# Optimization experiments

Measured on AMD Instinct MI355X. Metric: run time of the kernel, lower is better.

## Reference

```python
import jax, jax.numpy as jnp
import numpy as np

CUTOFF = 10.0
K = 32            # max_num_neighbors
NUM_GRAPHS = 64
ATOMS = 128
N = NUM_GRAPHS * ATOMS
HID = 128
FIL = 128
NG = 50           # num_gaussians
LAYERS = 6
MAX_Z = 100
PI = 3.14159265   # constant used verbatim in the torch source


def silu(x):
    return x * jax.nn.sigmoid(x)


def build_graph(pos, batch):
    """Dense cdist + per-node top-K neighbor selection (radius_graph_pure).
    Returns idx[i,k] = k-th nearest neighbor j of center i, and a validity mask.
    Torch edge (row, col) = (j, i): node j receives a message computed from x[i].
    """
    p = jax.lax.stop_gradient(pos)
    d2 = jnp.sum((p[:, None, :] - p[None, :, :]) ** 2, -1)          # [N,N]
    same = batch[:, None] == batch[None, :]
    eye = jnp.eye(p.shape[0], dtype=bool)
    valid = same & (d2 < CUTOFF * CUTOFF) & (~eye)
    dm = jnp.where(valid, d2, jnp.inf)
    neg, idx = jax.lax.top_k(-dm, K)                                 # [N,K]
    return idx, jnp.isfinite(neg)                                    # edge valid iff within mask


def setup_inputs() -> dict:
    key = jax.random.key(0)
    ks = jax.random.split(key, 20)
    s = 0.05
    inp = {
        "pos": jax.random.normal(ks[0], (N, 3), jnp.float32),
        "z": jax.random.randint(ks[1], (N,), 0, MAX_Z),
        "batch": jnp.repeat(jnp.arange(NUM_GRAPHS), ATOMS),
        # parameters (weights stored as [in, out])
        "emb": jax.random.normal(ks[2], (MAX_Z, HID), jnp.float32) * s,
        "mw1": jax.random.normal(ks[3], (LAYERS, NG, FIL), jnp.float32) * s,
        "mb1": jax.random.normal(ks[4], (LAYERS, FIL), jnp.float32) * s,
        "mw2": jax.random.normal(ks[5], (LAYERS, FIL, FIL), jnp.float32) * s,
        "mb2": jax.random.normal(ks[6], (LAYERS, FIL), jnp.float32) * s,
        "l1w": jax.random.normal(ks[7], (LAYERS, HID, FIL), jnp.float32) * s,
        "l1b": jax.random.normal(ks[8], (LAYERS, FIL), jnp.float32) * s,
        "l2w": jax.random.normal(ks[9], (LAYERS, FIL, HID), jnp.float32) * s,
        "l2b": jax.random.normal(ks[10], (LAYERS, HID), jnp.float32) * s,
        "ow1": jax.random.normal(ks[11], (HID, HID // 2), jnp.float32) * s,
        "ob1": jax.random.normal(ks[12], (HID // 2,), jnp.float32) * s,
        "ow2": jax.random.normal(ks[13], (HID // 2, 1), jnp.float32) * s,
        "ob2": jax.random.normal(ks[14], (1,), jnp.float32) * s,
    }
    return inp


def reference(pos, z, batch, emb, mw1, mb1, mw2, mb2, l1w, l1b, l2w, l2b, ow1, ob1, ow2, ob2):
    idx, evalid = build_graph(pos, batch)                 # [N,K], [N,K]
    ev = evalid.astype(pos.dtype)
    diff = pos[idx] - pos[:, None, :]                     # [N,K,3]
    d2e = jnp.sum(diff * diff, -1)
    dist = jnp.sqrt(jnp.where(evalid, d2e, 1.0))          # safe sqrt for masked edges
    offset = jnp.linspace(0.0, CUTOFF, NG)
    width = CUTOFF / (NG - 1)
    rbf = jnp.exp(-0.5 * ((dist[..., None] - offset) / width) ** 2)   # [N,K,NG]
    cval = 0.5 * (jnp.cos(dist * PI / CUTOFF) + 1.0)
    cval = cval * (dist < CUTOFF).astype(pos.dtype) * ev  # zero out invalid edges

    h = emb[z]                                            # [N,HID]
    flat_idx = idx.reshape(-1)                            # receivers (torch row)
    for l in range(LAYERS):
        W = silu(rbf @ mw1[l] + mb1[l]) @ mw2[l] + mb2[l]           # filter MLP
        W = W * cval[..., None]                                       # [N,K,FIL]
        xj = (h @ l1w[l] + l1b[l])[:, None, :]                        # sender = center i
        msg = (xj * W).reshape(N * K, FIL)
        agg = jax.ops.segment_sum(msg, flat_idx, num_segments=N)     # scatter_add at row
        h = h + silu(agg @ l2w[l] + l2b[l])

    out = (silu(h @ ow1 + ob1) @ ow2 + ob2)[:, 0]         # [N]
    return jax.ops.segment_sum(out, batch, num_segments=NUM_GRAPHS)  # [G]
```

## Files before the change

### kernel.cpp

```cpp
#include <hip/hip_runtime.h>
#include <math.h>

typedef unsigned short u16;
typedef unsigned int   u32;
typedef unsigned long long u64;

#define NATOMS 8192
#define GRAPHS 64
#define KNN    32
#define NGAUSS 50
#define HID    128
#define LAYERS 6
#define NTAB   4096
#define SA     136
#define SW1    72
#define SH     132

typedef __attribute__((ext_vector_type(8))) short bf16x8;
typedef __attribute__((ext_vector_type(4))) float f32x4;

__device__ __forceinline__ float bf2f(u16 v) {
    return __uint_as_float(((u32)v) << 16);
}
__device__ __forceinline__ u16 f2bf(float f) {
    u32 u = __float_as_uint(f);
    u32 lsb = (u >> 16) & 1u;
    u += 0x7fffu + lsb;
    return (u16)(u >> 16);
}
__device__ __forceinline__ u32 pkbf(float lo, float hi) {
#if __has_builtin(__builtin_amdgcn_cvt_pk_bf16_f32)
    auto r = __builtin_amdgcn_cvt_pk_bf16_f32(lo, hi);
    u32 u; __builtin_memcpy(&u, &r, 4); return u;
#else
    return (u32)f2bf(lo) | ((u32)f2bf(hi) << 16);
#endif
}
__device__ __forceinline__ float silu_f(float x) {
    return x * __builtin_amdgcn_rcpf(1.0f + __expf(-x));
}
__device__ __forceinline__ bf16x8 ldfrag(const u16* p) {
    return *(const bf16x8*)__builtin_assume_aligned(p, 16);
}
__device__ __forceinline__ u64 shfl_xor_u64(u64 v, int mask) {
    u32 lo = (u32)v, hi = (u32)(v >> 32);
    lo = (u32)__shfl_xor((int)lo, mask, 64);
    hi = (u32)__shfl_xor((int)hi, mask, 64);
    return ((u64)hi << 32) | lo;
}
__device__ __forceinline__ float ldf(const void* p, int i, bool f32in) {
    return f32in ? ((const float*)p)[i] : bf2f(((const u16*)p)[i]);
}
union U8 { bf16x8 v; u32 w[4]; };

__global__ void probe_kernel(const u16* __restrict__ raw, int* __restrict__ flag,
                             int* __restrict__ rev_cnt, float* __restrict__ gsum,
                             int* __restrict__ done_cnt, int* __restrict__ xflags) {
    __shared__ int s;
    int t = threadIdx.x;
    if (t == 0) s = 0;
    __syncthreads();
    float x = bf2f(raw[2 * t]);
    if (!(fabsf(x) < 1000.0f)) atomicOr(&s, 1);
    for (int i = t; i < NATOMS; i += 256) rev_cnt[i] = 0;
    for (int i = t; i < 2048; i += 256) xflags[i] = 0;
    if (t < GRAPHS) gsum[t] = 0.0f;
    if (t == 0) *done_cnt = 0;
    __syncthreads();
    if (t == 0) *flag = s;
}

#define NARR 9
struct IngestDesc {
    const void* src[NARR];
    void*       dst[NARR];
    int         n[NARR];
};

#define NB_BUILD 2048
#define NB_PREP  768

__launch_bounds__(256)
__global__ void setup_kernel(const void* __restrict__ pos,
                             const void* __restrict__ l1w, const void* __restrict__ l2w,
                             u16* __restrict__ l1wt, u16* __restrict__ l2wt,
                             IngestDesc d, int total_ing,
                             const int* __restrict__ flag,
                             int* __restrict__ rev_cnt, u32* __restrict__ rev) {
    int bid = blockIdx.x;
    bool f32in = (*flag != 0);
    if (bid < NB_BUILD) {
        int wv = threadIdx.x >> 6, lane = threadIdx.x & 63;
        int t = bid * 4 + wv;
        int tl = t & 127;
        int base = t & ~127;
        float cx = ldf(pos, t * 3 + 0, f32in);
        float cy = ldf(pos, t * 3 + 1, f32in);
        float cz = ldf(pos, t * 3 + 2, f32in);
        u64 key[2];
#pragma unroll
        for (int c = 0; c < 2; ++c) {
            int j = lane + c * 64;
            float jx = ldf(pos, (base + j) * 3 + 0, f32in);
            float jy = ldf(pos, (base + j) * 3 + 1, f32in);
            float jz = ldf(pos, (base + j) * 3 + 2, f32in);
            float dx = __fsub_rn(cx, jx);
            float dy = __fsub_rn(cy, jy);
            float dz = __fsub_rn(cz, jz);
            float d2 = __fadd_rn(__fadd_rn(__fmul_rn(dx, dx), __fmul_rn(dy, dy)),
                                 __fmul_rn(dz, dz));
            bool valid = (j != tl) && (d2 < 100.0f);
            key[c] = valid ? ((((u64)__float_as_uint(d2)) << 32) | (u32)j) : ~0ULL;
        }
#pragma unroll
        for (int k = 2; k <= 128; k <<= 1) {
#pragma unroll
            for (int j = k >> 1; j > 0; j >>= 1) {
                if (j == 64) {
                    u64 lo = key[0] < key[1] ? key[0] : key[1];
                    u64 hi = key[0] < key[1] ? key[1] : key[0];
                    key[0] = lo; key[1] = hi;
                } else {
#pragma unroll
                    for (int r = 0; r < 2; ++r) {
                        u64 o = shfl_xor_u64(key[r], j);
                        u32 ii = (u32)(r * 64 + lane);
                        bool dir = ((ii & (u32)k) == 0);
                        bool lower = ((ii & (u32)j) == 0);
                        bool keep_min = (dir == lower);
                        bool less = key[r] < o;
                        key[r] = (less == keep_min) ? key[r] : o;
                    }
                }
            }
        }
        if (lane < KNN) {
            u64 m = key[0];
            if (m != ~0ULL) {
                float d2 = __uint_as_float((u32)(m >> 32));
                float dd = __fsqrt_rn(d2);
                if (dd < 10.0f) {
                    float u = dd * ((float)(NTAB - 1) / 10.0f);
                    int i0 = (int)(u + 0.5f);
                    if (i0 > NTAB - 1) i0 = NTAB - 1;
                    int jn = base + (int)(m & 0xffffffffu);
                    int p = atomicAdd(&rev_cnt[jn], 1);
                    rev[(size_t)jn * 128 + p] = ((u32)i0 << 7) | (u32)(t & 127);
                }
            }
        }
    } else if (bid < NB_BUILD + NB_PREP) {
        int gid = (bid - NB_BUILD) * 256 + threadIdx.x;
        int seg = gid / 98304;
        int tt = gid % 98304;
        int l = tt >> 14;
        int n = (tt >> 7) & 127;
        int k = tt & 127;
        const void* src = (seg == 0) ? l1w : l2w;
        u16* dst = (seg == 0) ? l1wt : l2wt;
        int si = l * 16384 + k * 128 + n;
        float v = f32in ? ((const float*)src)[si] : bf2f(((const u16*)src)[si]);
        dst[tt] = f2bf(v);
    } else {
        int gid = (bid - NB_BUILD - NB_PREP) * 256 + threadIdx.x;
        if (gid < total_ing) {
            int a = 0, off = gid;
            while (off >= d.n[a]) { off -= d.n[a]; ++a; }
            float v = f32in ? ((const float*)d.src[a])[off]
                            : bf2f(((const u16*)d.src[a])[off]);
            ((float*)d.dst[a])[off] = v;
        }
    }
}

__launch_bounds__(256)
__global__ void vtab_kernel(const void* __restrict__ mw1,
                            const void* __restrict__ mw2,
                            const float* __restrict__ b1,
                            const float* __restrict__ b2,
                            const int* __restrict__ flag,
                            u32* __restrict__ pk) {
    __shared__ u16 s_t1[128 * SA];
    __shared__ u16 s_w1[128 * SW1];
    __shared__ u16 s_w2[128 * SA];
    int tid = threadIdx.x;
    int l = blockIdx.x / (NTAB / 128);
    int rbase = (blockIdx.x % (NTAB / 128)) * 128;
    {
        bool f32in = (*flag != 0);
#pragma unroll
        for (int p = 0; p < 32; ++p) {
            int idx = p * 256 + tid;
            int k = idx >> 7, n = idx & 127;
            float v = (k < 50) ? ldf(mw1, l * 6400 + k * 128 + n, f32in) : 0.0f;
            s_w1[n * SW1 + k] = f2bf(v);
        }
#pragma unroll
        for (int p = 0; p < 64; ++p) {
            int idx = p * 256 + tid;
            int k = idx >> 7, n = idx & 127;
            s_w2[n * SA + k] = f2bf(ldf(mw2, l * 16384 + k * 128 + n, f32in));
        }
    }
    __syncthreads();

    int wv = tid >> 6, lane = tid & 63;
    int quad = lane >> 4, lr = lane & 15;
    int m0 = wv * 32;

    {
        const float wgi = 49.0f / 10.0f;
        const float dstep = 10.0f / (float)(NTAB - 1);
        U8 afr[2][2];
#pragma unroll
        for (int mt = 0; mt < 2; ++mt) {
            float d = (float)(rbase + m0 + mt * 16 + lr) * dstep;
            float u = d * wgi;
#pragma unroll
            for (int kki = 0; kki < 2; ++kki) {
                float t0 = u - (float)(quad * 8) - (float)(kki * 32);
                float vj[8];
#pragma unroll
                for (int j = 0; j < 8; ++j) {
                    float tt = t0 - (float)j;
                    float e = __expf(-0.5f * tt * tt);
                    if (kki == 1 && (quad * 8 + j) >= 18) e = 0.0f;
                    vj[j] = e;
                }
#pragma unroll
                for (int p = 0; p < 4; ++p)
                    afr[mt][kki].w[p] = pkbf(vj[2 * p], vj[2 * p + 1]);
            }
        }
        f32x4 accA[2][8];
#pragma unroll
        for (int mt = 0; mt < 2; ++mt)
#pragma unroll
            for (int nt = 0; nt < 8; ++nt) accA[mt][nt] = (f32x4){0.f, 0.f, 0.f, 0.f};
#pragma unroll
        for (int kki = 0; kki < 2; ++kki) {
#pragma unroll
            for (int nt = 0; nt < 8; ++nt) {
                bf16x8 b = ldfrag(&s_w1[(nt * 16 + lr) * SW1 + kki * 32 + quad * 8]);
                accA[0][nt] = __builtin_amdgcn_mfma_f32_16x16x32_bf16(afr[0][kki].v, b, accA[0][nt], 0, 0, 0);
                accA[1][nt] = __builtin_amdgcn_mfma_f32_16x16x32_bf16(afr[1][kki].v, b, accA[1][nt], 0, 0, 0);
            }
        }
#pragma unroll
        for (int mt = 0; mt < 2; ++mt) {
            int r0 = m0 + mt * 16 + quad * 4;
            u16* tp0 = &s_t1[r0 * SA + lr];
#pragma unroll
            for (int nt = 0; nt < 8; ++nt) {
                int col = nt * 16;
                float bb = b1[l * 128 + col + lr];
                u32 p01 = pkbf(silu_f(accA[mt][nt][0] + bb),
                               silu_f(accA[mt][nt][1] + bb));
                u32 p23 = pkbf(silu_f(accA[mt][nt][2] + bb),
                               silu_f(accA[mt][nt][3] + bb));
                u16* tp = tp0 + col;
                tp[0]      = (u16)p01;
                tp[SA]     = (u16)(p01 >> 16);
                tp[2 * SA] = (u16)p23;
                tp[3 * SA] = (u16)(p23 >> 16);
            }
        }
    }
    {
        f32x4 accB[2][8];
#pragma unroll
        for (int mt = 0; mt < 2; ++mt)
#pragma unroll
            for (int nt = 0; nt < 8; ++nt) accB[mt][nt] = (f32x4){0.f, 0.f, 0.f, 0.f};
#pragma unroll
        for (int kk = 0; kk < 128; kk += 32) {
            bf16x8 a0 = ldfrag(&s_t1[(m0 + lr)      * SA + kk + quad * 8]);
            bf16x8 a1 = ldfrag(&s_t1[(m0 + 16 + lr) * SA + kk + quad * 8]);
#pragma unroll
            for (int nt = 0; nt < 8; ++nt) {
                bf16x8 b = ldfrag(&s_w2[(nt * 16 + lr) * SA + kk + quad * 8]);
                accB[0][nt] = __builtin_amdgcn_mfma_f32_16x16x32_bf16(a0, b, accB[0][nt], 0, 0, 0);
                accB[1][nt] = __builtin_amdgcn_mfma_f32_16x16x32_bf16(a1, b, accB[1][nt], 0, 0, 0);
            }
        }
        const float dstep = 10.0f / (float)(NTAB - 1);
#pragma unroll
        for (int mt = 0; mt < 2; ++mt) {
            int r0 = m0 + mt * 16 + quad * 4;
            float cv[4];
#pragma unroll
            for (int r = 0; r < 4; ++r) {
                float d = (float)(rbase + r0 + r) * dstep;
                cv[r] = 0.5f * (cosf(d * 3.14159265f / 10.0f) + 1.0f);
            }
#pragma unroll
            for (int nt = 0; nt < 8; ++nt) {
                int col = nt * 16 + lr;
                float bb = b2[l * 128 + col];
#pragma unroll
                for (int r = 0; r < 4; ++r) {
                    float val = (accB[mt][nt][r] + bb) * cv[r];
                    float oth = __shfl_xor(val, 1, 64);
                    if ((lr & 1) == 0) {
                        int row = rbase + r0 + r;
                        pk[((size_t)l * NTAB + row) * 64 + (col >> 1)] =
                            pkbf(val, oth);
                    }
                }
            }
        }
    }
}

#define AGG_ISSUE(T, X, base, ev)                                              \
    {                                                                          \
        _Pragma("unroll") for (int q = 0; q < 8; ++q) {                        \
            int e = (base) + q;                                                \
            u32 pe = __builtin_amdgcn_readlane((ev), e & 63);                  \
            int sy = (int)(pe >> 7);                                           \
            int sx = (int)(pe & 127u);                                         \
            T[q] = pkl[(size_t)sy * 64 + lane];                                \
            X[q] = *(const u32*)&s_x[sx * SA + c2];                            \
        }                                                                      \
    }

#define AGG_COMPUTE(T, X)                                                      \
    {                                                                          \
        _Pragma("unroll") for (int q = 0; q < 8; ++q) {                        \
            float v0 = bf2f((u16)T[q]) * bf2f((u16)X[q]);                      \
            float v1 = bf2f((u16)(T[q] >> 16)) * bf2f((u16)(X[q] >> 16));      \
            switch (q & 3) {                                                   \
                case 0: a0 += v0; a1 += v1; break;                             \
                case 1: b0 += v0; b1v += v1; break;                            \
                case 2: c0 += v0; c1 += v1; break;                             \
                default: d0 += v0; d1 += v1; break;                            \
            }                                                                  \
        }                                                                      \
    }

__launch_bounds__(1024, 1)
__global__ void graph_kernel(const int* __restrict__ rev_cnt,
                             const u32* __restrict__ rev,
                             const u32* __restrict__ pk,
                             const int* __restrict__ z,
                             const float* __restrict__ emb,
                             const u16* __restrict__ l1wt,
                             const float* __restrict__ l1b,
                             const u16* __restrict__ l2wt,
                             const float* __restrict__ l2b,
                             const float* __restrict__ ow1,
                             const float* __restrict__ ob1,
                             const float* __restrict__ ow2,
                             const float* __restrict__ ob2,
                             u32* __restrict__ xbuf,
                             int* __restrict__ xflags,
                             float* __restrict__ gsum,
                             int* __restrict__ done_cnt,
                             void* __restrict__ out,
                             const int* __restrict__ flag) {
    __shared__ __align__(16) u16 s_x[128 * SA];
    __shared__ __align__(16) u16 s_hb[64 * SA];
    __shared__ __align__(16) u16 s_pair[2 * 64 * SA];
    __shared__ float s_b1a[LAYERS * 128];
    __shared__ float s_b2a[LAYERS * 128];
    __shared__ float s_sum;
    __shared__ int s_last;

    u16* s_ahi = s_pair;
    u16* s_alo = s_pair + 64 * SA;

    int tid = threadIdx.x;
    int bid = blockIdx.x;
    int g = bid & 63, q4 = bid >> 6;
    int abase = g * 128;
    int rbase = q4 * 32;
    int w = tid >> 6, lane = tid & 63;
    int quad = lane >> 4, lr = lane & 15;
    int rowt = (w >> 3) * 16;
    int coln = (w & 7) * 16;
    int c2 = lane * 2;

    float hreg[4];

    for (int i = tid; i < LAYERS * 128; i += 1024) {
        s_b1a[i] = l1b[i];
        s_b2a[i] = l2b[i];
    }

    int j0 = abase + rbase + w * 2;
    int dgv[2];
    u32 eAv[2], eBv[2];
#pragma unroll
    for (int rr = 0; rr < 2; ++rr) {
        int j = j0 + rr;
        dgv[rr] = rev_cnt[j];
        eAv[rr] = rev[(size_t)j * 128 + lane];
        eBv[rr] = (dgv[rr] > 64) ? rev[(size_t)j * 128 + 64 + lane] : eAv[rr];
    }

    {
        int r = tid >> 5, cb = (tid & 31) * 4;
        const float* src = emb + (size_t)z[abase + rbase + r] * 128 + cb;
        float4 v = *(const float4*)src;
        u32* dd = (u32*)&s_hb[r * SA + cb];
        dd[0] = pkbf(v.x, v.y); dd[1] = pkbf(v.z, v.w);
    }
    __syncthreads();

    {
        f32x4 acc = (f32x4){0.f, 0.f, 0.f, 0.f};
#pragma unroll
        for (int kk = 0; kk < 128; kk += 32) {
            bf16x8 a = ldfrag(&s_hb[(rowt + lr) * SA + kk + quad * 8]);
            bf16x8 b = ldfrag(l1wt + (coln + lr) * 128 + kk + quad * 8);
            acc = __builtin_amdgcn_mfma_f32_16x16x32_bf16(a, b, acc, 0, 0, 0);
        }
#pragma unroll
        for (int r = 0; r < 4; ++r) {
            int col = coln + lr;
            s_x[(rbase + rowt + quad * 4 + r) * SA + col] =
                f2bf(acc[r] + s_b1a[col]);
        }
    }

    for (int l = 0; l <= LAYERS; ++l) {
        if (l < LAYERS) {
            int e = l;
            u32* xbw = xbuf + ((size_t)bid * 2 + (e & 1)) * 2048;
            __syncthreads();
#pragma unroll
            for (int p = 0; p < 2; ++p) {
                int i = tid + p * 1024;
                int row = i >> 6, col = i & 63;
                u32 v = *(const u32*)&s_x[(rbase + row) * SA + col * 2];
                __hip_atomic_store(&xbw[i], v, __ATOMIC_RELAXED,
                                   __HIP_MEMORY_SCOPE_SYSTEM);
            }
            __syncthreads();
            if (tid == 0)
                __hip_atomic_store(&xflags[(g * 4 + q4) * 8 + e], 1,
                                   __ATOMIC_RELAXED, __HIP_MEMORY_SCOPE_SYSTEM);
            if (tid < 3) {
                int pq = (q4 + 1 + tid) & 3;
                const int* pf = &xflags[(g * 4 + pq) * 8 + e];
                while (__hip_atomic_load(pf, __ATOMIC_RELAXED,
                                         __HIP_MEMORY_SCOPE_SYSTEM) == 0)
                    __builtin_amdgcn_s_sleep(1);
            }
            __syncthreads();
#pragma unroll
            for (int k = 0; k < 3; ++k) {
                int pq = (q4 + 1 + k) & 3;
                const u32* xbr = xbuf + ((size_t)(g + 64 * pq) * 2 + (e & 1)) * 2048;
#pragma unroll
                for (int p = 0; p < 2; ++p) {
                    int i = tid + p * 1024;
                    int row = i >> 6, col = i & 63;
                    u32 v = __hip_atomic_load(&xbr[i], __ATOMIC_RELAXED,
                                              __HIP_MEMORY_SCOPE_SYSTEM);
                    *(u32*)&s_x[(pq * 32 + row) * SA + col * 2] = v;
                }
            }
            __syncthreads();
        }
        if (l == LAYERS) break;

        const u32* pkl = pk + (size_t)l * NTAB * 64;

#pragma unroll
        for (int rr = 0; rr < 2; ++rr) {
            int row = w * 2 + rr;
            int deg = dgv[rr];
            u32 e0 = eAv[rr];
            u32 e1 = eBv[rr];
            float a0 = 0.f, a1 = 0.f, b0 = 0.f, b1v = 0.f;
            float c0 = 0.f, c1 = 0.f, d0 = 0.f, d1 = 0.f;
            u32 tA[8], xA[8], tB[8], xB[8];
            int ng = deg >> 3;
            if (ng > 0) {
                AGG_ISSUE(tA, xA, 0, e0);
                int gi = 1;
                for (; gi + 1 < ng; gi += 2) {
                    u32 evB = (gi < 8) ? e0 : e1;
                    AGG_ISSUE(tB, xB, gi * 8, evB);
                    AGG_COMPUTE(tA, xA);
                    u32 evA = ((gi + 1) < 8) ? e0 : e1;
                    AGG_ISSUE(tA, xA, (gi + 1) * 8, evA);
                    AGG_COMPUTE(tB, xB);
                }
                if (gi < ng) {
                    u32 evB = (gi < 8) ? e0 : e1;
                    AGG_ISSUE(tB, xB, gi * 8, evB);
                    AGG_COMPUTE(tA, xA);
                    AGG_COMPUTE(tB, xB);
                } else {
                    AGG_COMPUTE(tA, xA);
                }
            }
            for (int it = ng * 8; it < deg; ++it) {
                u32 ev = (it < 64) ? e0 : e1;
                u32 pe = __builtin_amdgcn_readlane(ev, it & 63);
                int sy = (int)(pe >> 7);
                int sx = (int)(pe & 127u);
                u32 t = pkl[(size_t)sy * 64 + lane];
                u32 x = *(const u32*)&s_x[sx * SA + c2];
                a0 += bf2f((u16)t) * bf2f((u16)x);
                a1 += bf2f((u16)(t >> 16)) * bf2f((u16)(x >> 16));
            }
            float sxv = (a0 + b0) + (c0 + d0);
            float syv = (a1 + b1v) + (c1 + d1);
            u32 hp = pkbf(sxv, syv);
            u32 lp = pkbf(sxv - bf2f((u16)hp), syv - bf2f((u16)(hp >> 16)));
            *(u32*)&s_ahi[row * SA + c2] = hp;
            *(u32*)&s_alo[row * SA + c2] = lp;
        }
        __syncthreads();

        {
            const u16* B2t = l2wt + (size_t)l * 16384;
            f32x4 acc = (f32x4){0.f, 0.f, 0.f, 0.f};
#pragma unroll
            for (int kk = 0; kk < 128; kk += 32) {
                bf16x8 ah = ldfrag(&s_ahi[(rowt + lr) * SA + kk + quad * 8]);
                bf16x8 al = ldfrag(&s_alo[(rowt + lr) * SA + kk + quad * 8]);
                bf16x8 b = ldfrag(B2t + (coln + lr) * 128 + kk + quad * 8);
                acc = __builtin_amdgcn_mfma_f32_16x16x32_bf16(ah, b, acc, 0, 0, 0);
                acc = __builtin_amdgcn_mfma_f32_16x16x32_bf16(al, b, acc, 0, 0, 0);
            }
            if (l == LAYERS - 1 && tid == 0) s_sum = 0.0f;
            int col = coln + lr;
#pragma unroll
            for (int r = 0; r < 4; ++r) {
                int row = rowt + quad * 4 + r;
                float hold = (l == 0)
                    ? emb[(size_t)z[abase + rbase + row] * 128 + col]
                    : hreg[r];
                float hn = hold + silu_f(acc[r] + s_b2a[l * 128 + col]);
                hreg[r] = hn;
                if (l < LAYERS - 1) s_hb[row * SA + col] = f2bf(hn);
            }
        }
        __syncthreads();

        if (l < LAYERS - 1) {
            const u16* B1n = l1wt + (size_t)(l + 1) * 16384;
            f32x4 ac2 = (f32x4){0.f, 0.f, 0.f, 0.f};
#pragma unroll
            for (int kk = 0; kk < 128; kk += 32) {
                bf16x8 a = ldfrag(&s_hb[(rowt + lr) * SA + kk + quad * 8]);
                bf16x8 b = ldfrag(B1n + (coln + lr) * 128 + kk + quad * 8);
                ac2 = __builtin_amdgcn_mfma_f32_16x16x32_bf16(a, b, ac2, 0, 0, 0);
            }
            int col = coln + lr;
#pragma unroll
            for (int r = 0; r < 4; ++r) {
                s_x[(rbase + rowt + quad * 4 + r) * SA + col] =
                    f2bf(ac2[r] + s_b1a[(l + 1) * 128 + col]);
            }
        } else {
            float* s_hf = (float*)s_pair;
            float* s_w  = (float*)s_x;
            {
                float4* dst = (float4*)s_w;
                const float4* src4 = (const float4*)ow1;
                dst[tid] = src4[tid];
                dst[tid + 1024] = src4[tid + 1024];
            }
#pragma unroll
            for (int r = 0; r < 4; ++r)
                s_hf[(rowt + quad * 4 + r) * SH + coln + lr] = hreg[r];
            __syncthreads();
            int atom = tid >> 5, cg = tid & 31;
            const float* hr = &s_hf[atom * SH];
            float ax = 0.f, ay = 0.f;
#pragma unroll 8
            for (int f = 0; f < 128; ++f) {
                float hv = hr[f];
                float2 wv = ((const float2*)&s_w[f * 64])[cg];
                ax += hv * wv.x; ay += hv * wv.y;
            }
            int c0i = cg * 2;
            float v = silu_f(ax + ob1[c0i + 0]) * ow2[c0i + 0]
                    + silu_f(ay + ob1[c0i + 1]) * ow2[c0i + 1];
            v += __shfl_xor(v, 1, 64);
            v += __shfl_xor(v, 2, 64);
            v += __shfl_xor(v, 4, 64);
            v += __shfl_xor(v, 8, 64);
            v += __shfl_xor(v, 16, 64);
            if ((tid & 31) == 0) atomicAdd(&s_sum, v + ob2[0]);
            __syncthreads();
            if (tid == 0) {
                atomicAdd(&gsum[g], s_sum);
                __threadfence();
                int tk = __hip_atomic_fetch_add(done_cnt, 1, __ATOMIC_ACQ_REL,
                                                __HIP_MEMORY_SCOPE_AGENT);
                s_last = (tk == 4 * GRAPHS - 1);
            }
            __syncthreads();
            if (s_last && tid < GRAPHS) {
                float gg = __hip_atomic_load(&gsum[tid], __ATOMIC_RELAXED,
                                             __HIP_MEMORY_SCOPE_AGENT);
                if (*flag) ((float*)out)[tid] = gg;
                else       ((u16*)out)[tid]   = f2bf(gg);
            }
            break;
        }
    }
}

extern "C" void kernel_launch(void* const* d_in, const int* in_sizes, int n_in,
                              void* d_out, int out_size, void* d_ws, size_t ws_size,
                              hipStream_t stream) {
    const void* pos  = d_in[0];
    const int*  z    = (const int*)d_in[1];
    const void* emb  = d_in[3];
    const void* mw1  = d_in[4];
    const void* mb1  = d_in[5];
    const void* mw2  = d_in[6];
    const void* mb2  = d_in[7];
    const void* l1w  = d_in[8];
    const void* l1b  = d_in[9];
    const void* l2w  = d_in[10];
    const void* l2b  = d_in[11];
    const void* ow1  = d_in[12];
    const void* ob1  = d_in[13];
    const void* ow2  = d_in[14];
    const void* ob2  = d_in[15];

    char* ws = (char*)d_ws;
    const size_t KB = 1024, MB = 1048576;
    int*   w_flag  = (int*)  (ws);
    int*   w_done  = (int*)  (ws + 64);
    int*   w_xfl   = (int*)  (ws + 8 * KB);
    float* c_emb   = (float*)(ws + 112 * KB);
    float* c_mb1   = (float*)(ws + 168 * KB);
    float* c_mb2   = (float*)(ws + 176 * KB);
    float* c_l1b   = (float*)(ws + 184 * KB);
    float* c_l2b   = (float*)(ws + 192 * KB);
    float* c_ow1   = (float*)(ws + 200 * KB);
    float* c_ob1   = (float*)(ws + 236 * KB);
    float* c_ow2   = (float*)(ws + 240 * KB);
    float* c_ob2   = (float*)(ws + 244 * KB);
    float* w_gsum  = (float*)(ws + 248 * KB);
    u16*   c_l1wt  = (u16*)  (ws + 256 * KB);
    u16*   c_l2wt  = (u16*)  (ws + 448 * KB);
    int*   rev_cnt = (int*)  (ws + 2  * MB);
    u32*   w_rev   = (u32*)  (ws + 3  * MB);
    u32*   w_pk    = (u32*)  (ws + 21 * MB);
    u32*   w_xbuf  = (u32*)  (ws + 28 * MB);

    probe_kernel<<<1, 256, 0, stream>>>((const u16*)emb, w_flag, rev_cnt,
                                        w_gsum, w_done, w_xfl);

    IngestDesc dsc;
    const void* srcs[NARR] = {emb, mb1, mb2, l1b, l2b, ow1, ob1, ow2, ob2};
    void* dsts[NARR] = {c_emb, c_mb1, c_mb2, c_l1b, c_l2b, c_ow1, c_ob1,
                        c_ow2, c_ob2};
    int ns_[NARR] = {12800, 768, 768, 768, 768, 8192, 64, 64, 1};
    int total = 0;
    for (int a = 0; a < NARR; ++a) {
        dsc.src[a] = srcs[a]; dsc.dst[a] = dsts[a]; dsc.n[a] = ns_[a];
        total += ns_[a];
    }
    int nb_ing = (total + 255) / 256;
    setup_kernel<<<NB_BUILD + NB_PREP + nb_ing, 256, 0, stream>>>(
        pos, l1w, l2w, c_l1wt, c_l2wt, dsc, total, w_flag, rev_cnt, w_rev);

    vtab_kernel<<<LAYERS * NTAB / 128, 256, 0, stream>>>(
        mw1, mw2, c_mb1, c_mb2, w_flag, w_pk);

    graph_kernel<<<4 * GRAPHS, 1024, 0, stream>>>(
        rev_cnt, w_rev, w_pk, z, c_emb, c_l1wt, c_l1b, c_l2wt, c_l2b,
        c_ow1, c_ob1, c_ow2, c_ob2, w_xbuf, w_xfl,
        w_gsum, w_done, d_out, w_flag);
}
```

Baseline: 244.7 us.

## Balance per-wave aggregation load by degree-sorted row pairing; widen xbuf exchange to 64-bit

Each block sorts its 32 destination rows by in-degree with a wave-level bitonic sort, then gives each wave one high-degree and one low-degree row so the aggregation work per wave evens out. The cross-block exchange of the x tile through global memory switches from two 32-bit atomic stores and loads per thread to a single 64-bit one. The sort adds a little setup and an extra barrier dependency, and the paired rows are no longer contiguous.

```diff
diff --git a/kernel.cpp b/kernel.cpp
--- a/kernel.cpp
+++ b/kernel.cpp
@@ -363,6 +363,7 @@
     __shared__ __align__(16) u16 s_pair[2 * 64 * SA];
     __shared__ float s_b1a[LAYERS * 128];
     __shared__ float s_b2a[LAYERS * 128];
+    __shared__ int s_perm[32];
     __shared__ float s_sum;
     __shared__ int s_last;
 
@@ -387,15 +388,25 @@
         s_b2a[i] = l2b[i];
     }
 
-    int j0 = abase + rbase + w * 2;
-    int dgv[2];
-    u32 eAv[2], eBv[2];
-#pragma unroll
-    for (int rr = 0; rr < 2; ++rr) {
-        int j = j0 + rr;
-        dgv[rr] = rev_cnt[j];
-        eAv[rr] = rev[(size_t)j * 128 + lane];
-        eBv[rr] = (dgv[rr] > 64) ? rev[(size_t)j * 128 + 64 + lane] : eAv[rr];
+    if (w == 0) {
+        u32 key = 0;
+        if (lane < 32) {
+            int dg = rev_cnt[abase + rbase + lane];
+            key = ((u32)dg << 8) | (u32)lane;
+        }
+#pragma unroll
+        for (int k = 2; k <= 64; k <<= 1) {
+#pragma unroll
+            for (int j = k >> 1; j > 0; j >>= 1) {
+                u32 o = (u32)__shfl_xor((int)key, j, 64);
+                bool dir = ((lane & k) == 0);
+                bool lower = ((lane & j) == 0);
+                bool keep_max = (dir == lower);
+                bool greater = key > o;
+                key = (greater == keep_max) ? key : o;
+            }
+        }
+        if (lane < 32) s_perm[lane] = (int)(key & 0xffu);
     }
 
     {
@@ -407,6 +418,19 @@
     }
     __syncthreads();
 
+    int rloc[2];
+    rloc[0] = s_perm[w];
+    rloc[1] = s_perm[31 - w];
+    int dgv[2];
+    u32 eAv[2], eBv[2];
+#pragma unroll
+    for (int rr = 0; rr < 2; ++rr) {
+        int j = abase + rbase + rloc[rr];
+        dgv[rr] = rev_cnt[j];
+        eAv[rr] = rev[(size_t)j * 128 + lane];
+        eBv[rr] = (dgv[rr] > 64) ? rev[(size_t)j * 128 + 64 + lane] : eAv[rr];
+    }
+
     {
         f32x4 acc = (f32x4){0.f, 0.f, 0.f, 0.f};
 #pragma unroll
@@ -426,14 +450,12 @@
     for (int l = 0; l <= LAYERS; ++l) {
         if (l < LAYERS) {
             int e = l;
-            u32* xbw = xbuf + ((size_t)bid * 2 + (e & 1)) * 2048;
+            u64* xbw = (u64*)(xbuf + ((size_t)bid * 2 + (e & 1)) * 2048);
             __syncthreads();
-#pragma unroll
-            for (int p = 0; p < 2; ++p) {
-                int i = tid + p * 1024;
-                int row = i >> 6, col = i & 63;
-                u32 v = *(const u32*)&s_x[(rbase + row) * SA + col * 2];
-                __hip_atomic_store(&xbw[i], v, __ATOMIC_RELAXED,
+            {
+                u64 v = *(const u64*)&s_x[(rbase + (tid >> 5)) * SA +
+                                          (tid & 31) * 4];
+                __hip_atomic_store(&xbw[tid], v, __ATOMIC_RELAXED,
                                    __HIP_MEMORY_SCOPE_SYSTEM);
             }
             __syncthreads();
@@ -451,15 +473,11 @@
 #pragma unroll
             for (int k = 0; k < 3; ++k) {
                 int pq = (q4 + 1 + k) & 3;
-                const u32* xbr = xbuf + ((size_t)(g + 64 * pq) * 2 + (e & 1)) * 2048;
-#pragma unroll
-                for (int p = 0; p < 2; ++p) {
-                    int i = tid + p * 1024;
-                    int row = i >> 6, col = i & 63;
-                    u32 v = __hip_atomic_load(&xbr[i], __ATOMIC_RELAXED,
-                                              __HIP_MEMORY_SCOPE_SYSTEM);
-                    *(u32*)&s_x[(pq * 32 + row) * SA + col * 2] = v;
-                }
+                const u64* xbr = (const u64*)(xbuf +
+                    ((size_t)(g + 64 * pq) * 2 + (e & 1)) * 2048);
+                u64 v = __hip_atomic_load(&xbr[tid], __ATOMIC_RELAXED,
+                                          __HIP_MEMORY_SCOPE_SYSTEM);
+                *(u64*)&s_x[(pq * 32 + (tid >> 5)) * SA + (tid & 31) * 4] = v;
             }
             __syncthreads();
         }
@@ -469,7 +487,7 @@
 
 #pragma unroll
         for (int rr = 0; rr < 2; ++rr) {
-            int row = w * 2 + rr;
+            int row = rloc[rr];
             int deg = dgv[rr];
             u32 e0 = eAv[rr];
             u32 e1 = eBv[rr];
```

Result: faster. 233.6 us (-4.6%).

## Split each graph across eight blocks instead of four in graph kernel

Applied to the files above, without the earlier changes.

The persistent graph kernel now uses 512 blocks, eight per graph, each owning 16 receiver atoms, so every wave handles one receiver row instead of two. The per-layer cross-block exchange of projected features goes through global buffers and flags with seven peers, using 64-bit stores and loads. The aim is to spread work over more compute units and shorten each block's serial aggregation. In exchange, half the waves sit idle during the MFMA stages, and inter-block flag synchronisation grows. Spin-waiting on peer blocks also relies on all 512 blocks being resident at the same time.

```diff
diff --git a/kernel.cpp b/kernel.cpp
--- a/kernel.cpp
+++ b/kernel.cpp
@@ -63,7 +63,7 @@
     float x = bf2f(raw[2 * t]);
     if (!(fabsf(x) < 1000.0f)) atomicOr(&s, 1);
     for (int i = t; i < NATOMS; i += 256) rev_cnt[i] = 0;
-    for (int i = t; i < 2048; i += 256) xflags[i] = 0;
+    for (int i = t; i < 4096; i += 256) xflags[i] = 0;
     if (t < GRAPHS) gsum[t] = 0.0f;
     if (t == 0) *done_cnt = 0;
     __syncthreads();
@@ -338,7 +338,7 @@
         }                                                                      \
     }
 
-__launch_bounds__(1024, 1)
+__launch_bounds__(1024, 8)
 __global__ void graph_kernel(const int* __restrict__ rev_cnt,
                              const u32* __restrict__ rev,
                              const u32* __restrict__ pk,
@@ -359,24 +359,23 @@
                              void* __restrict__ out,
                              const int* __restrict__ flag) {
     __shared__ __align__(16) u16 s_x[128 * SA];
-    __shared__ __align__(16) u16 s_hb[64 * SA];
-    __shared__ __align__(16) u16 s_pair[2 * 64 * SA];
+    __shared__ __align__(16) u16 s_hb[16 * SA];
+    __shared__ __align__(16) u16 s_pair[2 * 16 * SA];
     __shared__ float s_b1a[LAYERS * 128];
     __shared__ float s_b2a[LAYERS * 128];
     __shared__ float s_sum;
     __shared__ int s_last;
 
     u16* s_ahi = s_pair;
-    u16* s_alo = s_pair + 64 * SA;
+    u16* s_alo = s_pair + 16 * SA;
 
     int tid = threadIdx.x;
     int bid = blockIdx.x;
-    int g = bid & 63, q4 = bid >> 6;
+    int g = bid & 63, oct = bid >> 6;
     int abase = g * 128;
-    int rbase = q4 * 32;
+    int rbase = oct * 16;
     int w = tid >> 6, lane = tid & 63;
     int quad = lane >> 4, lr = lane & 15;
-    int rowt = (w >> 3) * 16;
     int coln = (w & 7) * 16;
     int c2 = lane * 2;
 
@@ -387,18 +386,12 @@
         s_b2a[i] = l2b[i];
     }
 
-    int j0 = abase + rbase + w * 2;
-    int dgv[2];
-    u32 eAv[2], eBv[2];
-#pragma unroll
-    for (int rr = 0; rr < 2; ++rr) {
-        int j = j0 + rr;
-        dgv[rr] = rev_cnt[j];
-        eAv[rr] = rev[(size_t)j * 128 + lane];
-        eBv[rr] = (dgv[rr] > 64) ? rev[(size_t)j * 128 + 64 + lane] : eAv[rr];
-    }
-
-    {
+    int jrecv = abase + rbase + w;
+    int deg0 = rev_cnt[jrecv];
+    u32 eA0 = rev[(size_t)jrecv * 128 + lane];
+    u32 eB0 = (deg0 > 64) ? rev[(size_t)jrecv * 128 + 64 + lane] : eA0;
+
+    if (tid < 512) {
         int r = tid >> 5, cb = (tid & 31) * 4;
         const float* src = emb + (size_t)z[abase + rbase + r] * 128 + cb;
         float4 v = *(const float4*)src;
@@ -407,58 +400,53 @@
     }
     __syncthreads();
 
-    {
+    if (w < 8) {
         f32x4 acc = (f32x4){0.f, 0.f, 0.f, 0.f};
 #pragma unroll
         for (int kk = 0; kk < 128; kk += 32) {
-            bf16x8 a = ldfrag(&s_hb[(rowt + lr) * SA + kk + quad * 8]);
+            bf16x8 a = ldfrag(&s_hb[lr * SA + kk + quad * 8]);
             bf16x8 b = ldfrag(l1wt + (coln + lr) * 128 + kk + quad * 8);
             acc = __builtin_amdgcn_mfma_f32_16x16x32_bf16(a, b, acc, 0, 0, 0);
         }
 #pragma unroll
         for (int r = 0; r < 4; ++r) {
             int col = coln + lr;
-            s_x[(rbase + rowt + quad * 4 + r) * SA + col] =
-                f2bf(acc[r] + s_b1a[col]);
+            s_x[(rbase + quad * 4 + r) * SA + col] = f2bf(acc[r] + s_b1a[col]);
         }
     }
 
     for (int l = 0; l <= LAYERS; ++l) {
         if (l < LAYERS) {
             int e = l;
-            u32* xbw = xbuf + ((size_t)bid * 2 + (e & 1)) * 2048;
+            u64* xbw = (u64*)(xbuf + ((size_t)bid * 2 + (e & 1)) * 1024);
             __syncthreads();
-#pragma unroll
-            for (int p = 0; p < 2; ++p) {
-                int i = tid + p * 1024;
-                int row = i >> 6, col = i & 63;
-                u32 v = *(const u32*)&s_x[(rbase + row) * SA + col * 2];
-                __hip_atomic_store(&xbw[i], v, __ATOMIC_RELAXED,
+            if (tid < 512) {
+                u64 v = *(const u64*)&s_x[(rbase + (tid >> 5)) * SA +
+                                          (tid & 31) * 4];
+                __hip_atomic_store(&xbw[tid], v, __ATOMIC_RELAXED,
                                    __HIP_MEMORY_SCOPE_SYSTEM);
             }
             __syncthreads();
             if (tid == 0)
-                __hip_atomic_store(&xflags[(g * 4 + q4) * 8 + e], 1,
+                __hip_atomic_store(&xflags[(g * 8 + oct) * 8 + e], 1,
                                    __ATOMIC_RELAXED, __HIP_MEMORY_SCOPE_SYSTEM);
-            if (tid < 3) {
-                int pq = (q4 + 1 + tid) & 3;
-                const int* pf = &xflags[(g * 4 + pq) * 8 + e];
+            if (tid < 7) {
+                int pq = (oct + 1 + tid) & 7;
+                const int* pf = &xflags[(g * 8 + pq) * 8 + e];
                 while (__hip_atomic_load(pf, __ATOMIC_RELAXED,
                                          __HIP_MEMORY_SCOPE_SYSTEM) == 0)
                     __builtin_amdgcn_s_sleep(1);
             }
             __syncthreads();
-#pragma unroll
-            for (int k = 0; k < 3; ++k) {
-                int pq = (q4 + 1 + k) & 3;
-                const u32* xbr = xbuf + ((size_t)(g + 64 * pq) * 2 + (e & 1)) * 2048;
-#pragma unroll
-                for (int p = 0; p < 2; ++p) {
-                    int i = tid + p * 1024;
-                    int row = i >> 6, col = i & 63;
-                    u32 v = __hip_atomic_load(&xbr[i], __ATOMIC_RELAXED,
+            if (tid < 512) {
+#pragma unroll
+                for (int k = 0; k < 7; ++k) {
+                    int pq = (oct + 1 + k) & 7;
+                    const u64* xbr = (const u64*)(xbuf +
+                        ((size_t)(g + 64 * pq) * 2 + (e & 1)) * 1024);
+                    u64 v = __hip_atomic_load(&xbr[tid], __ATOMIC_RELAXED,
                                               __HIP_MEMORY_SCOPE_SYSTEM);
-                    *(u32*)&s_x[(pq * 32 + row) * SA + col * 2] = v;
+                    *(u64*)&s_x[(pq * 16 + (tid >> 5)) * SA + (tid & 31) * 4] = v;
                 }
             }
             __syncthreads();
@@ -467,12 +455,11 @@
 
         const u32* pkl = pk + (size_t)l * NTAB * 64;
 
-#pragma unroll
-        for (int rr = 0; rr < 2; ++rr) {
-            int row = w * 2 + rr;
-            int deg = dgv[rr];
-            u32 e0 = eAv[rr];
-            u32 e1 = eBv[rr];
+        {
+            int row = w;
+            int deg = deg0;
+            u32 e0 = eA0;
+            u32 e1 = eB0;
             float a0 = 0.f, a1 = 0.f, b0 = 0.f, b1v = 0.f;
             float c0 = 0.f, c1 = 0.f, d0 = 0.f, d1 = 0.f;
             u32 tA[8], xA[8], tB[8], xB[8];
@@ -516,22 +503,21 @@
         }
         __syncthreads();
 
-        {
+        if (w < 8) {
             const u16* B2t = l2wt + (size_t)l * 16384;
             f32x4 acc = (f32x4){0.f, 0.f, 0.f, 0.f};
 #pragma unroll
             for (int kk = 0; kk < 128; kk += 32) {
-                bf16x8 ah = ldfrag(&s_ahi[(rowt + lr) * SA + kk + quad * 8]);
-                bf16x8 al = ldfrag(&s_alo[(rowt + lr) * SA + kk + quad * 8]);
+                bf16x8 ah = ldfrag(&s_ahi[lr * SA + kk + quad * 8]);
+                bf16x8 al = ldfrag(&s_alo[lr * SA + kk + quad * 8]);
                 bf16x8 b = ldfrag(B2t + (coln + lr) * 128 + kk + quad * 8);
                 acc = __builtin_amdgcn_mfma_f32_16x16x32_bf16(ah, b, acc, 0, 0, 0);
                 acc = __builtin_amdgcn_mfma_f32_16x16x32_bf16(al, b, acc, 0, 0, 0);
             }
-            if (l == LAYERS - 1 && tid == 0) s_sum = 0.0f;
             int col = coln + lr;
 #pragma unroll
             for (int r = 0; r < 4; ++r) {
-                int row = rowt + quad * 4 + r;
+                int row = quad * 4 + r;
                 float hold = (l == 0)
                     ? emb[(size_t)z[abase + rbase + row] * 128 + col]
                     : hreg[r];
@@ -540,22 +526,25 @@
                 if (l < LAYERS - 1) s_hb[row * SA + col] = f2bf(hn);
             }
         }
+        if (l == LAYERS - 1 && tid == 0) s_sum = 0.0f;
         __syncthreads();
 
         if (l < LAYERS - 1) {
-            const u16* B1n = l1wt + (size_t)(l + 1) * 16384;
-            f32x4 ac2 = (f32x4){0.f, 0.f, 0.f, 0.f};
-#pragma unroll
-            for (int kk = 0; kk < 128; kk += 32) {
-                bf16x8 a = ldfrag(&s_hb[(rowt + lr) * SA + kk + quad * 8]);
-                bf16x8 b = ldfrag(B1n + (coln + lr) * 128 + kk + quad * 8);
-                ac2 = __builtin_amdgcn_mfma_f32_16x16x32_bf16(a, b, ac2, 0, 0, 0);
-            }
-            int col = coln + lr;
-#pragma unroll
-            for (int r = 0; r < 4; ++r) {
-                s_x[(rbase + rowt + quad * 4 + r) * SA + col] =
-                    f2bf(ac2[r] + s_b1a[(l + 1) * 128 + col]);
+            if (w < 8) {
+                const u16* B1n = l1wt + (size_t)(l + 1) * 16384;
+                f32x4 ac2 = (f32x4){0.f, 0.f, 0.f, 0.f};
+#pragma unroll
+                for (int kk = 0; kk < 128; kk += 32) {
+                    bf16x8 a = ldfrag(&s_hb[lr * SA + kk + quad * 8]);
+                    bf16x8 b = ldfrag(B1n + (coln + lr) * 128 + kk + quad * 8);
+                    ac2 = __builtin_amdgcn_mfma_f32_16x16x32_bf16(a, b, ac2, 0, 0, 0);
+                }
+                int col = coln + lr;
+#pragma unroll
+                for (int r = 0; r < 4; ++r) {
+                    s_x[(rbase + quad * 4 + r) * SA + col] =
+                        f2bf(ac2[r] + s_b1a[(l + 1) * 128 + col]);
+                }
             }
         } else {
             float* s_hf = (float*)s_pair;
@@ -566,35 +555,32 @@
                 dst[tid] = src4[tid];
                 dst[tid + 1024] = src4[tid + 1024];
             }
-#pragma unroll
-            for (int r = 0; r < 4; ++r)
-                s_hf[(rowt + quad * 4 + r) * SH + coln + lr] = hreg[r];
+            if (w < 8) {
+#pragma unroll
+                for (int r = 0; r < 4; ++r)
+                    s_hf[(quad * 4 + r) * SH + coln + lr] = hreg[r];
+            }
             __syncthreads();
-            int atom = tid >> 5, cg = tid & 31;
-            const float* hr = &s_hf[atom * SH];
-            float ax = 0.f, ay = 0.f;
+            const float* hr = &s_hf[w * SH];
+            float ax = 0.f;
 #pragma unroll 8
-            for (int f = 0; f < 128; ++f) {
-                float hv = hr[f];
-                float2 wv = ((const float2*)&s_w[f * 64])[cg];
-                ax += hv * wv.x; ay += hv * wv.y;
-            }
-            int c0i = cg * 2;
-            float v = silu_f(ax + ob1[c0i + 0]) * ow2[c0i + 0]
-                    + silu_f(ay + ob1[c0i + 1]) * ow2[c0i + 1];
+            for (int f = 0; f < 128; ++f)
+                ax += hr[f] * s_w[f * 64 + lane];
+            float v = silu_f(ax + ob1[lane]) * ow2[lane];
             v += __shfl_xor(v, 1, 64);
             v += __shfl_xor(v, 2, 64);
             v += __shfl_xor(v, 4, 64);
             v += __shfl_xor(v, 8, 64);
             v += __shfl_xor(v, 16, 64);
-            if ((tid & 31) == 0) atomicAdd(&s_sum, v + ob2[0]);
+            v += __shfl_xor(v, 32, 64);
+            if (lane == 0) atomicAdd(&s_sum, v + ob2[0]);
             __syncthreads();
             if (tid == 0) {
                 atomicAdd(&gsum[g], s_sum);
                 __threadfence();
                 int tk = __hip_atomic_fetch_add(done_cnt, 1, __ATOMIC_ACQ_REL,
                                                 __HIP_MEMORY_SCOPE_AGENT);
-                s_last = (tk == 4 * GRAPHS - 1);
+                s_last = (tk == 8 * GRAPHS - 1);
             }
             __syncthreads();
             if (s_last && tid < GRAPHS) {
@@ -669,7 +655,7 @@
     vtab_kernel<<<LAYERS * NTAB / 128, 256, 0, stream>>>(
         mw1, mw2, c_mb1, c_mb2, w_flag, w_pk);
 
-    graph_kernel<<<4 * GRAPHS, 1024, 0, stream>>>(
+    graph_kernel<<<8 * GRAPHS, 1024, 0, stream>>>(
         rev_cnt, w_rev, w_pk, z, c_emb, c_l1wt, c_l1b, c_l2wt, c_l2b,
         c_ow1, c_ob1, c_ow2, c_ob2, w_xbuf, w_xfl,
         w_gsum, w_done, d_out, w_flag);
```

New measurement: 299.7 us. 22.4% more time.
